# Optimization experiments

Measured on AMD Instinct MI355X. Metric: run time of the kernel, lower is better.

Reference implementation:

```python
import jax, jax.numpy as jnp
import numpy as np

N, K, D = 20000, 32, 128


def setup_inputs() -> dict:
    key = jax.random.key(0)
    ks = jax.random.split(key, 10)
    return {
        "self_feats": jax.random.normal(ks[0], (N, D), jnp.float32),
        "self_vecs": jax.random.normal(ks[1], (N, D), jnp.float32),
        "neigh_vecs": jax.random.normal(ks[2], (N, K, D), jnp.float32),
        "link_vecs": jax.random.normal(ks[3], (N, K, D), jnp.float32),
        # selection probabilities kept away from 0 to avoid huge 1/p values
        "select_probs": jax.random.uniform(ks[4], (N, K), jnp.float32, 0.1, 1.0),
        "gate_self_w": jax.random.normal(ks[5], (D,), jnp.float32) * (1.0 / np.sqrt(D)),
        "gate_neigh_w": jax.random.normal(ks[6], (D,), jnp.float32) * (1.0 / np.sqrt(D)),
        "gate_link_w": jax.random.normal(ks[7], (D,), jnp.float32) * (1.0 / np.sqrt(D)),
        "self_weights": jax.random.normal(ks[8], (D, D), jnp.float32) * (1.0 / np.sqrt(D)),
        "link_weights": jax.random.normal(ks[9], (D, D), jnp.float32) * (1.0 / np.sqrt(D)),
    }


def reference(self_feats, self_vecs, neigh_vecs, link_vecs, select_probs,
              gate_self_w, gate_neigh_w, gate_link_w, self_weights, link_weights):
    # Gate: scalar-per-(node, neighbor) sigmoid gate. dropout=0, no gate bias.
    trans_self = self_vecs @ gate_self_w                       # [N]
    trans_neigh = jnp.einsum('nkd,d->nk', neigh_vecs, gate_neigh_w)  # [N,K]
    trans_link = jnp.einsum('nkd,d->nk', link_vecs, gate_link_w)     # [N,K]
    gate = jax.nn.sigmoid(trans_self[:, None] + trans_neigh + trans_link)  # [N,K]

    # Link-conditioned channel amplification
    trans_links = jax.nn.sigmoid(jnp.einsum('nkd,de->nke', link_vecs, link_weights))  # [N,K,D]
    trans_self_feats = self_feats @ self_weights                                      # [N,D]

    amplified = neigh_vecs * trans_links * trans_self_feats[:, None, :]               # [N,K,D]

    # select_probs is not None branch: importance-weighted mean over neighbors
    gate_div_prob = gate / select_probs                                               # [N,K]
    sum_neighs = jnp.mean(amplified * gate_div_prob[..., None], axis=-2)              # [N,D]

    return jax.nn.relu(sum_neighs)
```

## Files before the change

### kernel.cpp

```cpp
#include <hip/hip_runtime.h>
#include <stdint.h>

#define N_NODES 20000
#define K_NB 32
#define D_DIM 128

typedef short bf16x8 __attribute__((ext_vector_type(8)));
typedef float f32x4 __attribute__((ext_vector_type(4)));

__device__ __forceinline__ unsigned short f2bf(float f) {
    union { float f; unsigned u; } v; v.f = f;
    unsigned r = v.u + 0x7FFFu + ((v.u >> 16) & 1u);
    return (unsigned short)(r >> 16);
}

__device__ __forceinline__ bf16x8 pack8(float4 a, float4 b) {
    bf16x8 r;
    r[0] = (short)f2bf(a.x); r[1] = (short)f2bf(a.y);
    r[2] = (short)f2bf(a.z); r[3] = (short)f2bf(a.w);
    r[4] = (short)f2bf(b.x); r[5] = (short)f2bf(b.y);
    r[6] = (short)f2bf(b.z); r[7] = (short)f2bf(b.w);
    return r;
}

__device__ __forceinline__ float dot16(float4 a0, float4 a1, float4 a2, float4 a3,
                                       float4 b0, float4 b1, float4 b2, float4 b3) {
    return a0.x*b0.x + a0.y*b0.y + a0.z*b0.z + a0.w*b0.w
         + a1.x*b1.x + a1.y*b1.y + a1.z*b1.z + a1.w*b1.w
         + a2.x*b2.x + a2.y*b2.y + a2.z*b2.z + a2.w*b2.w
         + a3.x*b3.x + a3.y*b3.y + a3.z*b3.z + a3.w*b3.w;
}

__device__ __forceinline__ float sigm(float x) {
    return __builtin_amdgcn_rcpf(1.0f + __expf(-x));
}

#define A_STRIDE 136
#define NG_STRIDE 132

__global__ __launch_bounds__(256) void precompute_kernel(
    const float* __restrict__ self_feats,
    const float* __restrict__ self_vecs,
    const float* __restrict__ gate_self_w,
    const float* __restrict__ self_weights,
    float* __restrict__ tsf,
    float* __restrict__ ts)
{
    __shared__ __align__(16) unsigned short A[32 * A_STRIDE];

    const int tid  = threadIdx.x;
    const int lane = tid & 63;
    const int w    = tid >> 6;
    const int q    = lane >> 4;
    const int el   = lane & 15;
    const int row  = tid >> 3;
    const int seg  = tid & 7;
    const int node0 = blockIdx.x * 32;

    bf16x8 wf[2][4];
#pragma unroll
    for (int nt = 0; nt < 2; ++nt) {
        int e = 32 * w + 16 * nt + el;
#pragma unroll
        for (int s = 0; s < 4; ++s) {
#pragma unroll
            for (int j = 0; j < 8; ++j) {
                int d = 32 * s + 8 * q + j;
                wf[nt][s][j] = (short)f2bf(self_weights[d * 128 + e]);
            }
        }
    }

    const float4* gs = (const float4*)(gate_self_w + seg * 16);
    float4 g0 = gs[0], g1 = gs[1], g2 = gs[2], g3 = gs[3];

    {
        const float4* sfr = (const float4*)(self_feats + (size_t)(node0 + row) * 128 + seg * 16);
        float4 v0 = sfr[0], v1 = sfr[1], v2 = sfr[2], v3 = sfr[3];
        const float4* svr = (const float4*)(self_vecs + (size_t)(node0 + row) * 128 + seg * 16);
        float4 u0 = svr[0], u1 = svr[1], u2 = svr[2], u3 = svr[3];

        float part = dot16(u0, u1, u2, u3, g0, g1, g2, g3);
        part += __shfl_xor(part, 1);
        part += __shfl_xor(part, 2);
        part += __shfl_xor(part, 4);
        if (seg == 0) ts[node0 + row] = part;

        *(bf16x8*)&A[row * A_STRIDE + seg * 16]     = pack8(v0, v1);
        *(bf16x8*)&A[row * A_STRIDE + seg * 16 + 8] = pack8(v2, v3);
    }
    __syncthreads();

    bf16x8 af[2][4];
#pragma unroll
    for (int mt = 0; mt < 2; ++mt)
#pragma unroll
        for (int s = 0; s < 4; ++s)
            af[mt][s] = *(const bf16x8*)&A[(16 * mt + el) * A_STRIDE + 32 * s + 8 * q];

    f32x4 acc[2][2] = {};
#pragma unroll
    for (int mt = 0; mt < 2; ++mt)
#pragma unroll
        for (int nt = 0; nt < 2; ++nt)
#pragma unroll
            for (int s = 0; s < 4; ++s)
                acc[mt][nt] = __builtin_amdgcn_mfma_f32_16x16x32_bf16(
                    af[mt][s], wf[nt][s], acc[mt][nt], 0, 0, 0);

#pragma unroll
    for (int mt = 0; mt < 2; ++mt)
#pragma unroll
        for (int nt = 0; nt < 2; ++nt)
#pragma unroll
            for (int r = 0; r < 4; ++r) {
                int m = 16 * mt + 4 * q + r;
                tsf[(size_t)(node0 + m) * 128 + 32 * w + 16 * nt + el] = acc[mt][nt][r];
            }
}

__global__ __launch_bounds__(256) void aggregate_kernel(
    const float* __restrict__ neigh_vecs,
    const float* __restrict__ link_vecs,
    const float* __restrict__ select_probs,
    const float* __restrict__ gate_neigh_w,
    const float* __restrict__ gate_link_w,
    const float* __restrict__ link_weights,
    const float* __restrict__ tsf,
    const float* __restrict__ ts,
    float* __restrict__ out)
{
    __shared__ __align__(16) unsigned short A[32 * A_STRIDE];
    __shared__ __align__(16) float NG[32 * NG_STRIDE];
    __shared__ float tl_s[32], tn_s[32], gdp_s[32], tsf_s[128];

    const int tid  = threadIdx.x;
    const int lane = tid & 63;
    const int w    = tid >> 6;
    const int q    = lane >> 4;
    const int el   = lane & 15;
    const int row  = tid >> 3;
    const int seg  = tid & 7;

    bf16x8 wf[2][4];
#pragma unroll
    for (int nt = 0; nt < 2; ++nt) {
        int e = 32 * w + 16 * nt + el;
#pragma unroll
        for (int s = 0; s < 4; ++s) {
#pragma unroll
            for (int j = 0; j < 8; ++j) {
                int d = 32 * s + 8 * q + j;
                wf[nt][s][j] = (short)f2bf(link_weights[d * 128 + e]);
            }
        }
    }

    const float4* glp = (const float4*)(gate_link_w + seg * 16);
    float4 gl0 = glp[0], gl1 = glp[1], gl2 = glp[2], gl3 = glp[3];
    const float4* gnp = (const float4*)(gate_neigh_w + seg * 16);
    float4 gn0 = gnp[0], gn1 = gnp[1], gn2 = gnp[2], gn3 = gnp[3];

    for (int n = blockIdx.x; n < N_NODES; n += gridDim.x) {
        __syncthreads();

        float p_pref = 1.0f, ts_pref = 0.0f;
        if (tid < 32) {
            p_pref  = select_probs[(size_t)n * 32 + tid];
            ts_pref = ts[n];
        }
        if (tid < 128) tsf_s[tid] = tsf[(size_t)n * 128 + tid];

        const float4* lr = (const float4*)(link_vecs + ((size_t)n * 32 + row) * 128 + seg * 16);
        float4 v0 = lr[0], v1 = lr[1], v2 = lr[2], v3 = lr[3];
        const float4* nr = (const float4*)(neigh_vecs + ((size_t)n * 32 + row) * 128 + seg * 16);
        float4 u0 = nr[0], u1 = nr[1], u2 = nr[2], u3 = nr[3];

        float tl = dot16(v0, v1, v2, v3, gl0, gl1, gl2, gl3);
        tl += __shfl_xor(tl, 1);
        tl += __shfl_xor(tl, 2);
        tl += __shfl_xor(tl, 4);
        float tn = dot16(u0, u1, u2, u3, gn0, gn1, gn2, gn3);
        tn += __shfl_xor(tn, 1);
        tn += __shfl_xor(tn, 2);
        tn += __shfl_xor(tn, 4);
        if (seg == 0) { tl_s[row] = tl; tn_s[row] = tn; }

        *(bf16x8*)&A[row * A_STRIDE + seg * 16]     = pack8(v0, v1);
        *(bf16x8*)&A[row * A_STRIDE + seg * 16 + 8] = pack8(v2, v3);

        float4* ngp = (float4*)&NG[row * NG_STRIDE + seg * 16];
        ngp[0] = u0; ngp[1] = u1; ngp[2] = u2; ngp[3] = u3;

        __syncthreads();

        if (tid < 32) {
            float g = sigm(ts_pref + tn_s[tid] + tl_s[tid]);
            gdp_s[tid] = g / (p_pref * 32.0f);
        }

        bf16x8 af[2][4];
#pragma unroll
        for (int mt = 0; mt < 2; ++mt)
#pragma unroll
            for (int s = 0; s < 4; ++s)
                af[mt][s] = *(const bf16x8*)&A[(16 * mt + el) * A_STRIDE + 32 * s + 8 * q];

        f32x4 acc[2][2] = {};
#pragma unroll
        for (int mt = 0; mt < 2; ++mt)
#pragma unroll
            for (int nt = 0; nt < 2; ++nt)
#pragma unroll
                for (int s = 0; s < 4; ++s)
                    acc[mt][nt] = __builtin_amdgcn_mfma_f32_16x16x32_bf16(
                        af[mt][s], wf[nt][s], acc[mt][nt], 0, 0, 0);

        __syncthreads();

#pragma unroll
        for (int nt = 0; nt < 2; ++nt) {
            int c0 = 32 * w + 16 * nt;
            float s = 0.0f;
#pragma unroll
            for (int mt = 0; mt < 2; ++mt)
#pragma unroll
                for (int r = 0; r < 4; ++r) {
                    int m = 16 * mt + 4 * q + r;
                    float t = sigm(acc[mt][nt][r]);
                    s += t * NG[m * NG_STRIDE + c0 + el] * gdp_s[m];
                }
            s += __shfl_xor(s, 16);
            s += __shfl_xor(s, 32);
            if (q == 0) {
                float o = tsf_s[c0 + el] * s;
                out[(size_t)n * 128 + c0 + el] = o > 0.0f ? o : 0.0f;
            }
        }
    }
}

extern "C" void kernel_launch(void* const* d_in, const int* in_sizes, int n_in,
                              void* d_out, int out_size, void* d_ws, size_t ws_size,
                              hipStream_t stream) {
    const float* self_feats   = (const float*)d_in[0];
    const float* self_vecs    = (const float*)d_in[1];
    const float* neigh_vecs   = (const float*)d_in[2];
    const float* link_vecs    = (const float*)d_in[3];
    const float* select_probs = (const float*)d_in[4];
    const float* gate_self_w  = (const float*)d_in[5];
    const float* gate_neigh_w = (const float*)d_in[6];
    const float* gate_link_w  = (const float*)d_in[7];
    const float* self_weights = (const float*)d_in[8];
    const float* link_weights = (const float*)d_in[9];
    float* out = (float*)d_out;

    float* tsf = (float*)d_ws;
    float* ts  = tsf + (size_t)N_NODES * D_DIM;

    precompute_kernel<<<N_NODES / 32, 256, 0, stream>>>(
        self_feats, self_vecs, gate_self_w, self_weights, tsf, ts);
    aggregate_kernel<<<1024, 256, 0, stream>>>(
        neigh_vecs, link_vecs, select_probs, gate_neigh_w, gate_link_w,
        link_weights, tsf, ts, out);
}
```

Baseline: 690.7 us.

## Prefetch next node's inputs into registers and cut per-node barriers

The aggregate loop now loads the next node's link/neighbor rows, select probs, ts and tsf into registers while the current node's MFMA and reduction run. This software-pipelines global loads and hides memory latency. The gate is computed per thread from a combined shared t_s and reciprocal prob array rather than a serial tid<32 step, and tsf is kept in registers, which removes one barrier per iteration. The cost is more register pressure, which may lower occupancy.

```diff
diff --git a/kernel.cpp b/kernel.cpp
--- a/kernel.cpp
+++ b/kernel.cpp
@@ -132,7 +132,8 @@
 {
     __shared__ __align__(16) unsigned short A[32 * A_STRIDE];
     __shared__ __align__(16) float NG[32 * NG_STRIDE];
-    __shared__ float tl_s[32], tn_s[32], gdp_s[32], tsf_s[128];
+    __shared__ float t_s[32];
+    __shared__ float sp_s[32];
 
     const int tid  = threadIdx.x;
     const int lane = tid & 63;
@@ -161,21 +162,23 @@
     const float4* gnp = (const float4*)(gate_neigh_w + seg * 16);
     float4 gn0 = gnp[0], gn1 = gnp[1], gn2 = gnp[2], gn3 = gnp[3];
 
-    for (int n = blockIdx.x; n < N_NODES; n += gridDim.x) {
-        __syncthreads();
-
-        float p_pref = 1.0f, ts_pref = 0.0f;
-        if (tid < 32) {
-            p_pref  = select_probs[(size_t)n * 32 + tid];
-            ts_pref = ts[n];
-        }
-        if (tid < 128) tsf_s[tid] = tsf[(size_t)n * 128 + tid];
-
+    const int stride = gridDim.x;
+
+    float4 v0, v1, v2, v3, u0, u1, u2, u3;
+    float sp_r = 1.0f, ts_r = 0.0f, tsf_r0 = 0.0f, tsf_r1 = 0.0f;
+    {
+        int n = blockIdx.x;
         const float4* lr = (const float4*)(link_vecs + ((size_t)n * 32 + row) * 128 + seg * 16);
-        float4 v0 = lr[0], v1 = lr[1], v2 = lr[2], v3 = lr[3];
+        v0 = lr[0]; v1 = lr[1]; v2 = lr[2]; v3 = lr[3];
         const float4* nr = (const float4*)(neigh_vecs + ((size_t)n * 32 + row) * 128 + seg * 16);
-        float4 u0 = nr[0], u1 = nr[1], u2 = nr[2], u3 = nr[3];
-
+        u0 = nr[0]; u1 = nr[1]; u2 = nr[2]; u3 = nr[3];
+        if (tid < 32) sp_r = select_probs[(size_t)n * 32 + tid];
+        ts_r   = ts[n];
+        tsf_r0 = tsf[(size_t)n * 128 + 32 * w + el];
+        tsf_r1 = tsf[(size_t)n * 128 + 32 * w + 16 + el];
+    }
+
+    for (int n = blockIdx.x; n < N_NODES; n += stride) {
         float tl = dot16(v0, v1, v2, v3, gl0, gl1, gl2, gl3);
         tl += __shfl_xor(tl, 1);
         tl += __shfl_xor(tl, 2);
@@ -184,19 +187,29 @@
         tn += __shfl_xor(tn, 1);
         tn += __shfl_xor(tn, 2);
         tn += __shfl_xor(tn, 4);
-        if (seg == 0) { tl_s[row] = tl; tn_s[row] = tn; }
+        if (seg == 0) t_s[row] = tl + tn;
+        if (tid < 32) sp_s[tid] = __builtin_amdgcn_rcpf(32.0f * sp_r);
 
         *(bf16x8*)&A[row * A_STRIDE + seg * 16]     = pack8(v0, v1);
         *(bf16x8*)&A[row * A_STRIDE + seg * 16 + 8] = pack8(v2, v3);
-
         float4* ngp = (float4*)&NG[row * NG_STRIDE + seg * 16];
         ngp[0] = u0; ngp[1] = u1; ngp[2] = u2; ngp[3] = u3;
 
+        float ts_cur = ts_r, tc0 = tsf_r0, tc1 = tsf_r1;
+
         __syncthreads();
 
-        if (tid < 32) {
-            float g = sigm(ts_pref + tn_s[tid] + tl_s[tid]);
-            gdp_s[tid] = g / (p_pref * 32.0f);
+        {
+            int np = n + stride;
+            np = (np < N_NODES) ? np : n;
+            const float4* lr = (const float4*)(link_vecs + ((size_t)np * 32 + row) * 128 + seg * 16);
+            v0 = lr[0]; v1 = lr[1]; v2 = lr[2]; v3 = lr[3];
+            const float4* nr = (const float4*)(neigh_vecs + ((size_t)np * 32 + row) * 128 + seg * 16);
+            u0 = nr[0]; u1 = nr[1]; u2 = nr[2]; u3 = nr[3];
+            if (tid < 32) sp_r = select_probs[(size_t)np * 32 + tid];
+            ts_r   = ts[np];
+            tsf_r0 = tsf[(size_t)np * 128 + 32 * w + el];
+            tsf_r1 = tsf[(size_t)np * 128 + 32 * w + 16 + el];
         }
 
         bf16x8 af[2][4];
@@ -216,7 +229,14 @@
                     acc[mt][nt] = __builtin_amdgcn_mfma_f32_16x16x32_bf16(
                         af[mt][s], wf[nt][s], acc[mt][nt], 0, 0, 0);
 
-        __syncthreads();
+        float g[2][4];
+#pragma unroll
+        for (int mt = 0; mt < 2; ++mt)
+#pragma unroll
+            for (int r = 0; r < 4; ++r) {
+                int m = 16 * mt + 4 * q + r;
+                g[mt][r] = sigm(ts_cur + t_s[m]) * sp_s[m];
+            }
 
 #pragma unroll
         for (int nt = 0; nt < 2; ++nt) {
@@ -228,15 +248,18 @@
                 for (int r = 0; r < 4; ++r) {
                     int m = 16 * mt + 4 * q + r;
                     float t = sigm(acc[mt][nt][r]);
-                    s += t * NG[m * NG_STRIDE + c0 + el] * gdp_s[m];
+                    s += t * NG[m * NG_STRIDE + c0 + el] * g[mt][r];
                 }
             s += __shfl_xor(s, 16);
             s += __shfl_xor(s, 32);
             if (q == 0) {
-                float o = tsf_s[c0 + el] * s;
+                float tc = nt == 0 ? tc0 : tc1;
+                float o = tc * s;
                 out[(size_t)n * 128 + c0 + el] = o > 0.0f ? o : 0.0f;
             }
         }
+
+        __syncthreads();
     }
 }
 
```

New measurement: 654.3 us. -5.3%, faster.
